# Optimization experiments

Measured on AMD Instinct MI355X. Metric: run time of the kernel, lower is better.

## Reference

```python
import jax, jax.numpy as jnp
import numpy as np
import math

MAXL = 2
N = 256
TAU = 8


def _cg_coeff(j1, m1, j2, m2, J, M):
    if m1 + m2 != M or J < abs(j1 - j2) or J > j1 + j2:
        return 0.0
    f = math.factorial
    pre = math.sqrt((2 * J + 1) * f(J + j1 - j2) * f(J - j1 + j2) * f(j1 + j2 - J) / f(j1 + j2 + J + 1))
    pre *= math.sqrt(f(J + M) * f(J - M) * f(j1 - m1) * f(j1 + m1) * f(j2 - m2) * f(j2 + m2))
    kmin = max(0, j2 - J - m1, j1 + m2 - J)
    kmax = min(j1 + j2 - J, j1 - m1, j2 + m2)
    s = 0.0
    for k in range(kmin, kmax + 1):
        s += (-1.0) ** k / (f(k) * f(j1 + j2 - J - k) * f(j1 - m1 - k) * f(j2 + m2 - k) * f(J - j2 + m1 + k) * f(J - j1 - m2 + k))
    return pre * s


def _cg_tensor(l1, l2, L):
    C = np.zeros((2 * l1 + 1, 2 * l2 + 1, 2 * L + 1), np.float32)
    for m1 in range(-l1, l1 + 1):
        for m2 in range(-l2, l2 + 1):
            M = m1 + m2
            if -L <= M <= L:
                C[m1 + l1, m2 + l2, M + L] = _cg_coeff(l1, m1, l2, m2, L, M)
    return C

_CG = {}
for _l1 in range(MAXL + 1):
    for _l2 in range(MAXL + 1):
        for _L in range(abs(_l1 - _l2), min(_l1 + _l2, MAXL) + 1):
            _CG[(_l1, _l2, _L)] = _cg_tensor(_l1, _l2, _L)


def _cgproduct(xs, ys, maxl):
    # xs[l]: [..., 2l+1, tau_x], ys[l]: [..., 2l+1, tau_y]
    out = []
    for L in range(maxl + 1):
        chunks = []
        for l1 in range(maxl + 1):
            for l2 in range(maxl + 1):
                if abs(l1 - l2) <= L <= l1 + l2:
                    C = jnp.asarray(_CG[(l1, l2, L)])
                    t = jnp.einsum('...mc,...nd,mnM->...Mcd', xs[l1], ys[l2], C)
                    sh = t.shape
                    chunks.append(t.reshape(sh[:-2] + (sh[-2] * sh[-1],)))
        out.append(jnp.concatenate(chunks, axis=-1))
    return out


def _forward(v0, v1, v2, adj, s0, s1, s2, wn0, wn1, wn2, wr0, wr1, wr2):
    v = [v0, v1, v2]                       # [N, 1, 2l+1, tau]
    sph = [s0[None], s1[None], s2[None]]   # [1, N, N, 2l+1, 1]
    wn = [wn0, wn1, wn2]
    wr = [wr0, wr1, wr2]
    # message pass: gather/sum over neighbors (Rmask1 gather)
    vmp = [jnp.einsum('ij,jamc->iamc', adj, p)[None] for p in v]  # [1, N, 1, 2l+1, tau]
    # first CG product (vertex x vertex)
    cg_nl = _cgproduct(vmp, vmp, MAXL)
    # per-l channel mixing with weights_nl
    mixed = [jnp.einsum('bxymc,cd->bxymd', cg_nl[l], wn[l]) for l in range(MAXL + 1)]
    # repeat to pairwise adims [N, N] (broadcast over second array dim)
    n = adj.shape[0]
    rep = [jnp.broadcast_to(m, (1, n, n, m.shape[3], m.shape[4])) for m in mixed]
    # second CG product with relative-position spherical harmonics
    cg_rel = _cgproduct(rep, sph, MAXL)
    # per-cell mixing with weights_rel
    mixed_rel = [jnp.einsum('bxymc,xycd->bxymd', cg_rel[l], wr[l]) for l in range(MAXL + 1)]
    # sum over source-node array dim
    vsum = [jnp.sum(m, axis=1) for m in mixed_rel]  # [1, N, 2l+1, tau]
    # NormalizeVecArr mutates parts in place -> returned vertices_sum is normalized
    out = [p / jnp.sum(p) for p in vsum]
    # concatenate parts along m-axis for a single output array [1, N, 9, tau]
    return jnp.concatenate(out, axis=2)


def setup_inputs() -> dict:
    key = jax.random.key(0)
    ks = jax.random.split(key, 13)
    d = {}
    d['v0'] = jax.random.normal(ks[0], (N, 1, 1, TAU), jnp.float32)
    d['v1'] = jax.random.normal(ks[1], (N, 1, 3, TAU), jnp.float32)
    d['v2'] = jax.random.normal(ks[2], (N, 1, 5, TAU), jnp.float32)
    d['adj'] = jax.random.uniform(ks[3], (N, N), jnp.float32)
    d['s0'] = jax.random.normal(ks[4], (N, N, 1, 1), jnp.float32)
    d['s1'] = jax.random.normal(ks[5], (N, N, 3, 1), jnp.float32)
    d['s2'] = jax.random.normal(ks[6], (N, N, 5, 1), jnp.float32)
    W = 0.05
    d['wn0'] = W * jax.random.normal(ks[7], (192, TAU), jnp.float32)
    d['wn1'] = W * jax.random.normal(ks[8], (384, TAU), jnp.float32)
    d['wn2'] = W * jax.random.normal(ks[9], (384, TAU), jnp.float32)
    d['wr0'] = W * jax.random.normal(ks[10], (N, N, 24, TAU), jnp.float32)
    d['wr1'] = W * jax.random.normal(ks[11], (N, N, 48, TAU), jnp.float32)
    d['wr2'] = W * jax.random.normal(ks[12], (N, N, 48, TAU), jnp.float32)
    return d


def reference(v0, v1, v2, adj, s0, s1, s2, wn0, wn1, wn2, wr0, wr1, wr2):
    return _forward(v0, v1, v2, adj, s0, s1, s2, wn0, wn1, wn2, wr0, wr1, wr2)
```

## Files before the change

kernel.cpp:

```cpp
#include <hip/hip_runtime.h>

#define NN 256

#define C13  0.5773502691896258f
#define C15  0.4472135954999579f
#define CC12 0.7071067811865476f
#define S35  0.7745966692414834f
#define S310 0.5477225575051661f
#define C110 0.3162277660168379f
#define S25  0.6324555320336759f
#define S23  0.8164965809277260f
#define C16  0.4082482904638630f
#define S27  0.5345224838248488f
#define S37  0.6546536707079771f
#define C114 0.2672612419124244f

#define CGREL(mx, sv, r0, r1, r2) \
    r0[0] = mx[0]*sv[0]; \
    r0[1] = C13*(mx[1]*sv[3] - mx[2]*sv[2] + mx[3]*sv[1]); \
    r0[2] = C15*(mx[4]*sv[8] - mx[5]*sv[7] + mx[6]*sv[6] - mx[7]*sv[5] + mx[8]*sv[4]); \
    r1[0][0] = mx[0]*sv[1]; r1[1][0] = mx[0]*sv[2]; r1[2][0] = mx[0]*sv[3]; \
    r1[0][1] = mx[1]*sv[0]; r1[1][1] = mx[2]*sv[0]; r1[2][1] = mx[3]*sv[0]; \
    r1[0][2] = CC12*(mx[2]*sv[1] - mx[1]*sv[2]); \
    r1[1][2] = CC12*(mx[3]*sv[1] - mx[1]*sv[3]); \
    r1[2][2] = CC12*(mx[3]*sv[2] - mx[2]*sv[3]); \
    r1[0][3] = S35*mx[3]*sv[4] - S310*mx[2]*sv[5] + C110*mx[1]*sv[6]; \
    r1[1][3] = S310*(mx[3]*sv[5] + mx[1]*sv[7]) - S25*mx[2]*sv[6]; \
    r1[2][3] = S35*mx[1]*sv[8] - S310*mx[2]*sv[7] + C110*mx[3]*sv[6]; \
    r1[0][4] = C110*mx[6]*sv[1] - S310*mx[5]*sv[2] + S35*mx[4]*sv[3]; \
    r1[1][4] = S310*(mx[7]*sv[1] + mx[5]*sv[3]) - S25*mx[6]*sv[2]; \
    r1[2][4] = S35*mx[8]*sv[1] - S310*mx[7]*sv[2] + C110*mx[6]*sv[3]; \
    r1[0][5] = C15*(mx[7]*sv[4] - mx[4]*sv[7]) + S310*(mx[5]*sv[6] - mx[6]*sv[5]); \
    r1[1][5] = S25*(mx[8]*sv[4] - mx[4]*sv[8]) + C110*(mx[5]*sv[7] - mx[7]*sv[5]); \
    r1[2][5] = C15*(mx[8]*sv[5] - mx[5]*sv[8]) + S310*(mx[6]*sv[7] - mx[7]*sv[6]); \
    r2[0][0]=mx[0]*sv[4]; r2[1][0]=mx[0]*sv[5]; r2[2][0]=mx[0]*sv[6]; r2[3][0]=mx[0]*sv[7]; r2[4][0]=mx[0]*sv[8]; \
    r2[0][1] = mx[1]*sv[1]; \
    r2[1][1] = CC12*(mx[2]*sv[1] + mx[1]*sv[2]); \
    r2[2][1] = C16*(mx[3]*sv[1] + mx[1]*sv[3]) + S23*mx[2]*sv[2]; \
    r2[3][1] = CC12*(mx[3]*sv[2] + mx[2]*sv[3]); \
    r2[4][1] = mx[3]*sv[3]; \
    r2[0][2] = S23*mx[2]*sv[4] - C13*mx[1]*sv[5]; \
    r2[1][2] = C13*mx[3]*sv[4] + C16*mx[2]*sv[5] - CC12*mx[1]*sv[6]; \
    r2[2][2] = CC12*(mx[3]*sv[5] - mx[1]*sv[7]); \
    r2[3][2] = CC12*mx[3]*sv[6] - C16*mx[2]*sv[7] - C13*mx[1]*sv[8]; \
    r2[4][2] = C13*mx[3]*sv[7] - S23*mx[2]*sv[8]; \
    r2[0][3]=mx[4]*sv[0]; r2[1][3]=mx[5]*sv[0]; r2[2][3]=mx[6]*sv[0]; r2[3][3]=mx[7]*sv[0]; r2[4][3]=mx[8]*sv[0]; \
    r2[0][4] = C13*mx[5]*sv[1] - S23*mx[4]*sv[2]; \
    r2[1][4] = CC12*mx[6]*sv[1] - C16*mx[5]*sv[2] - C13*mx[4]*sv[3]; \
    r2[2][4] = CC12*(mx[7]*sv[1] - mx[5]*sv[3]); \
    r2[3][4] = C13*mx[8]*sv[1] + C16*mx[7]*sv[2] - CC12*mx[6]*sv[3]; \
    r2[4][4] = S23*mx[8]*sv[2] - C13*mx[7]*sv[3]; \
    r2[0][5] = S27*(mx[4]*sv[6] + mx[6]*sv[4]) - S37*mx[5]*sv[5]; \
    r2[1][5] = S37*(mx[4]*sv[7] + mx[7]*sv[4]) - C114*(mx[5]*sv[6] + mx[6]*sv[5]); \
    r2[2][5] = S27*(mx[8]*sv[4] + mx[4]*sv[8] - mx[6]*sv[6]) + C114*(mx[7]*sv[5] + mx[5]*sv[7]); \
    r2[3][5] = S37*(mx[8]*sv[5] + mx[5]*sv[8]) - C114*(mx[7]*sv[6] + mx[6]*sv[7]); \
    r2[4][5] = S27*(mx[8]*sv[6] + mx[6]*sv[8]) - S37*mx[7]*sv[7];

__global__ __launch_bounds__(256) void k_nodes(
                        const float* __restrict__ adj,
                        const float* __restrict__ v0,
                        const float* __restrict__ v1,
                        const float* __restrict__ v2,
                        const float* __restrict__ wn0,
                        const float* __restrict__ wn1,
                        const float* __restrict__ wn2,
                        float* __restrict__ mixed){
  __shared__ float part[4][72];
  int i = blockIdx.x;
  int tid = threadIdx.x, wv = tid >> 6, lane = tid & 63;

  {
    const float* vp1; int st1;
    if (lane < 8)       { vp1 = v0 + lane;      st1 = 8;  }
    else if (lane < 32) { vp1 = v1 + (lane-8);  st1 = 24; }
    else                { vp1 = v2 + (lane-32); st1 = 40; }
    const float* vp2 = v2 + 32 + lane;
    const float* arow = adj + i*NN;
    int j0 = wv*64;
    float a1a = 0.f, a1b = 0.f, a2a = 0.f, a2b = 0.f;
    #pragma unroll 8
    for (int j = j0; j < j0+64; j += 2){
      float av0 = arow[j], av1 = arow[j+1];
      a1a = fmaf(av0, vp1[j*st1], a1a);
      a1b = fmaf(av1, vp1[(j+1)*st1], a1b);
      if (lane < 8){
        a2a = fmaf(av0, vp2[j*40], a2a);
        a2b = fmaf(av1, vp2[(j+1)*40], a2b);
      }
    }
    part[wv][lane] = a1a + a1b;
    if (lane < 8) part[wv][64+lane] = a2a + a2b;
  }
  __syncthreads();
  if (wv) return;

  {
    float s = part[0][lane] + part[1][lane] + part[2][lane] + part[3][lane];
    float s2 = 0.f;
    if (lane < 8)
      s2 = part[0][64+lane] + part[1][64+lane] + part[2][64+lane] + part[3][64+lane];
    part[0][lane] = s;
    if (lane < 8) part[0][64+lane] = s2;
  }

  int c = lane >> 3, d = lane & 7;
  float mx[9], sv[9];
  #pragma unroll
  for (int j=0;j<9;j++){ mx[j] = part[0][j*8 + c]; sv[j] = part[0][j*8 + d]; }
  float r0[3], r1[3][6], r2[5][6];
  CGREL(mx, sv, r0, r1, r2)

  float a0[8], a1m[3][8], a2m[5][8];
  #pragma unroll
  for (int dp=0;dp<8;dp++){ a0[dp]=0.f;
    #pragma unroll
    for (int M=0;M<3;M++) a1m[M][dp]=0.f;
    #pragma unroll
    for (int M=0;M<5;M++) a2m[M][dp]=0.f;
  }
  #pragma unroll
  for (int k=0;k<3;k++){
    const float* row = wn0 + (k*64 + lane)*8;
    float4 u = *(const float4*)row;
    float4 v = *(const float4*)(row+4);
    float u8[8] = {u.x,u.y,u.z,u.w,v.x,v.y,v.z,v.w};
    #pragma unroll
    for (int dp=0;dp<8;dp++) a0[dp] = fmaf(r0[k], u8[dp], a0[dp]);
  }
  #pragma unroll
  for (int k=0;k<6;k++){
    const float* row = wn1 + (k*64 + lane)*8;
    float4 u = *(const float4*)row;
    float4 v = *(const float4*)(row+4);
    float u8[8] = {u.x,u.y,u.z,u.w,v.x,v.y,v.z,v.w};
    #pragma unroll
    for (int M=0;M<3;M++)
      #pragma unroll
      for (int dp=0;dp<8;dp++) a1m[M][dp] = fmaf(r1[M][k], u8[dp], a1m[M][dp]);
  }
  #pragma unroll
  for (int k=0;k<6;k++){
    const float* row = wn2 + (k*64 + lane)*8;
    float4 u = *(const float4*)row;
    float4 v = *(const float4*)(row+4);
    float u8[8] = {u.x,u.y,u.z,u.w,v.x,v.y,v.z,v.w};
    #pragma unroll
    for (int M=0;M<5;M++)
      #pragma unroll
      for (int dp=0;dp<8;dp++) a2m[M][dp] = fmaf(r2[M][k], u8[dp], a2m[M][dp]);
  }

  #pragma unroll
  for (int m=0;m<9;m++){
    #pragma unroll
    for (int dp=0;dp<8;dp++){
      float val = (m==0) ? a0[dp] : (m<4 ? a1m[m-1][dp] : a2m[m-4][dp]);
      val += __shfl_xor(val, 1);
      val += __shfl_xor(val, 2);
      val += __shfl_xor(val, 4);
      val += __shfl_xor(val, 8);
      val += __shfl_xor(val, 16);
      val += __shfl_xor(val, 32);
      if (lane == ((m*8+dp) & 63)) mixed[i*72 + m*8 + dp] = val;
    }
  }
}

#define XPW 8

#define LOAD_WR(x, W0, W1, W2) { \
  int pxy = (x)*NN + y; \
  const float* p0 = wr0 + pxy*192 + lane; \
  const float* p1 = wr1 + pxy*384 + lane; \
  const float* p2 = wr2 + pxy*384 + lane; \
  _Pragma("unroll") for (int k=0;k<3;k++) W0[k] = p0[k*64]; \
  _Pragma("unroll") for (int k=0;k<6;k++) W1[k] = p1[k*64]; \
  _Pragma("unroll") for (int k=0;k<6;k++) W2[k] = p2[k*64]; }

#define LOAD_MS(x) { \
  const float* mb = mixed + (x)*72 + cgp; \
  _Pragma("unroll") for (int j=0;j<9;j++) mx[j] = mb[j*8]; \
  int pxy = (x)*NN + y; \
  sv[0] = s0[pxy]; \
  _Pragma("unroll") for (int j=0;j<3;j++) sv[1+j] = s1[pxy*3+j]; \
  _Pragma("unroll") for (int j=0;j<5;j++) sv[4+j] = s2[pxy*5+j]; }

#define DO_FMA(W0, W1, W2) { \
  _Pragma("unroll") for (int k=0;k<3;k++) acc[0] = fmaf(r0[k], W0[k], acc[0]); \
  _Pragma("unroll") for (int k=0;k<6;k++){ \
    acc[1] = fmaf(r1[0][k], W1[k], acc[1]); \
    acc[2] = fmaf(r1[1][k], W1[k], acc[2]); \
    acc[3] = fmaf(r1[2][k], W1[k], acc[3]); \
    acc[4] = fmaf(r2[0][k], W2[k], acc[4]); \
    acc[5] = fmaf(r2[1][k], W2[k], acc[5]); \
    acc[6] = fmaf(r2[2][k], W2[k], acc[6]); \
    acc[7] = fmaf(r2[3][k], W2[k], acc[7]); \
    acc[8] = fmaf(r2[4][k], W2[k], acc[8]); } }

#define STEP(xw, WC0, WC1, WC2, WN0, WN1, WN2, xm) { \
  LOAD_WR(xw, WN0, WN1, WN2); \
  float r0[3], r1[3][6], r2[5][6]; \
  CGREL(mx, sv, r0, r1, r2) \
  LOAD_MS(xm); \
  DO_FMA(WC0, WC1, WC2); }

__global__ __launch_bounds__(256, 4) void k_pair(
    const float* __restrict__ mixed,
    const float* __restrict__ s0, const float* __restrict__ s1, const float* __restrict__ s2,
    const float* __restrict__ wr0, const float* __restrict__ wr1, const float* __restrict__ wr2,
    float* __restrict__ vsum){
  int tid = threadIdx.x;
  int lane = tid & 63;
  int w = blockIdx.x*4 + (tid>>6);
  int y = w & (NN-1);
  int xbase = (w >> 8) * XPW;
  int cgp = lane >> 3;
  int xlast = xbase + XPW - 1;

  float acc[9];
  #pragma unroll
  for (int m=0;m<9;m++) acc[m]=0.f;

  float mx[9], sv[9];
  float wA0[3], wA1[6], wA2[6], wB0[3], wB1[6], wB2[6];
  LOAD_MS(xbase);
  LOAD_WR(xbase, wA0, wA1, wA2);

  #pragma unroll
  for (int i=0;i<XPW;i+=2){
    int x1 = xbase + i + 1;
    int x2 = (i+2 < XPW) ? (xbase + i + 2) : xlast;
    STEP(x1, wA0, wA1, wA2, wB0, wB1, wB2, x1);
    STEP(x2, wB0, wB1, wB2, wA0, wA1, wA2, x2);
  }

  #pragma unroll
  for (int m=0;m<9;m++){
    float v = acc[m];
    v += __shfl_xor(v, 8);
    v += __shfl_xor(v, 16);
    v += __shfl_xor(v, 32);
    acc[m] = v;
  }
  if (lane < 8){
    #pragma unroll
    for (int m=0;m<9;m++) atomicAdd(&vsum[y*72 + m*8 + lane], acc[m]);
  }
}

__global__ void k_final(const float* __restrict__ vsum, float* __restrict__ out){
  __shared__ float ps[3];
  int t = threadIdx.x;
  if (t < 3) ps[t] = 0.f;
  __syncthreads();
  float vals[18];
  float p0=0.f, p1=0.f, p2=0.f;
  #pragma unroll
  for (int k=0;k<18;k++){
    int idx = t*18 + k;
    float v = vsum[idx];
    vals[k] = v;
    int mall = (idx >> 3) % 9;
    if (mall == 0) p0 += v; else if (mall < 4) p1 += v; else p2 += v;
  }
  #pragma unroll
  for (int s=1; s<64; s<<=1){
    p0 += __shfl_xor(p0, s);
    p1 += __shfl_xor(p1, s);
    p2 += __shfl_xor(p2, s);
  }
  if ((t & 63) == 0){
    atomicAdd(&ps[0], p0);
    atomicAdd(&ps[1], p1);
    atomicAdd(&ps[2], p2);
  }
  __syncthreads();
  float q0 = ps[0], q1 = ps[1], q2 = ps[2];
  #pragma unroll
  for (int k=0;k<18;k++){
    int idx = t*18 + k;
    int mall = (idx >> 3) % 9;
    float den = (mall == 0) ? q0 : (mall < 4 ? q1 : q2);
    out[idx] = vals[k] / den;
  }
}

extern "C" void kernel_launch(void* const* d_in, const int* in_sizes, int n_in,
                              void* d_out, int out_size, void* d_ws, size_t ws_size,
                              hipStream_t stream) {
  const float* v0  = (const float*)d_in[0];
  const float* v1  = (const float*)d_in[1];
  const float* v2  = (const float*)d_in[2];
  const float* adj = (const float*)d_in[3];
  const float* s0  = (const float*)d_in[4];
  const float* s1  = (const float*)d_in[5];
  const float* s2  = (const float*)d_in[6];
  const float* wn0 = (const float*)d_in[7];
  const float* wn1 = (const float*)d_in[8];
  const float* wn2 = (const float*)d_in[9];
  const float* wr0 = (const float*)d_in[10];
  const float* wr1 = (const float*)d_in[11];
  const float* wr2 = (const float*)d_in[12];
  float* out = (float*)d_out;

  float* ws    = (float*)d_ws;
  float* mixed = ws;
  float* vsum  = ws + 18432;

  hipMemsetAsync(vsum, 0, 18432*sizeof(float), stream);
  k_nodes<<<NN, 256, 0, stream>>>(adj, v0, v1, v2, wn0, wn1, wn2, mixed);
  k_pair<<<NN*(NN/XPW)/4, 256, 0, stream>>>(mixed, s0, s1, s2, wr0, wr1, wr2, vsum);
  k_final<<<1, 1024, 0, stream>>>(vsum, out);
}
```

Before: 83.83 us.

## Stream pair weights into a per-wave LDS ring via async global-to-LDS loads

Rewrites k_pair so each wave stages its mixed features, spherical harmonics and per-pair wr weights into shared memory with global_load_lds. The wr loads go through a three-deep ring buffer controlled by explicit vmcnt waits and scheduling barriers, replacing the register double-buffering. The aim is to keep more weight bytes in flight to hide the latency of this bandwidth-bound stream. In exchange it uses about 58KB of LDS per block, which limits occupancy, and drops the launch-bounds occupancy hint. It also depends on hand-counted waitcnt values and on LDS reads finishing before the async refills of the same slot.

```diff
diff --git a/kernel.cpp b/kernel.cpp
--- a/kernel.cpp
+++ b/kernel.cpp
@@ -1,6 +1,8 @@
 #include <hip/hip_runtime.h>
 
 #define NN 256
+#define XPW 8
+#define RING_D 3
 
 #define C13  0.5773502691896258f
 #define C15  0.4472135954999579f
@@ -56,6 +58,12 @@
     r2[3][5] = S37*(mx[8]*sv[5] + mx[5]*sv[8]) - C114*(mx[7]*sv[6] + mx[6]*sv[7]); \
     r2[4][5] = S27*(mx[8]*sv[6] + mx[6]*sv[8]) - S37*mx[7]*sv[7];
 
+typedef __attribute__((address_space(3))) unsigned       lds_u32_t;
+typedef __attribute__((address_space(1))) const unsigned glb_u32_t;
+__device__ __forceinline__ void gld4(const float* g, float* l){
+  __builtin_amdgcn_global_load_lds((glb_u32_t*)g, (lds_u32_t*)l, 4, 0, 0);
+}
+
 __global__ __launch_bounds__(256) void k_nodes(
                         const float* __restrict__ adj,
                         const float* __restrict__ v0,
@@ -68,7 +76,6 @@
   __shared__ float part[4][72];
   int i = blockIdx.x;
   int tid = threadIdx.x, wv = tid >> 6, lane = tid & 63;
-
   {
     const float* vp1; int st1;
     if (lane < 8)       { vp1 = v0 + lane;      st1 = 8;  }
@@ -93,7 +100,6 @@
   }
   __syncthreads();
   if (wv) return;
-
   {
     float s = part[0][lane] + part[1][lane] + part[2][lane] + part[3][lane];
     float s2 = 0.f;
@@ -102,7 +108,6 @@
     part[0][lane] = s;
     if (lane < 8) part[0][64+lane] = s2;
   }
-
   int c = lane >> 3, d = lane & 7;
   float mx[9], sv[9];
   #pragma unroll
@@ -149,7 +154,6 @@
       #pragma unroll
       for (int dp=0;dp<8;dp++) a2m[M][dp] = fmaf(r2[M][k], u8[dp], a2m[M][dp]);
   }
-
   #pragma unroll
   for (int m=0;m<9;m++){
     #pragma unroll
@@ -166,73 +170,99 @@
   }
 }
 
-#define XPW 8
-
-#define LOAD_WR(x, W0, W1, W2) { \
-  int pxy = (x)*NN + y; \
-  const float* p0 = wr0 + pxy*192 + lane; \
-  const float* p1 = wr1 + pxy*384 + lane; \
-  const float* p2 = wr2 + pxy*384 + lane; \
-  _Pragma("unroll") for (int k=0;k<3;k++) W0[k] = p0[k*64]; \
-  _Pragma("unroll") for (int k=0;k<6;k++) W1[k] = p1[k*64]; \
-  _Pragma("unroll") for (int k=0;k<6;k++) W2[k] = p2[k*64]; }
-
-#define LOAD_MS(x) { \
-  const float* mb = mixed + (x)*72 + cgp; \
-  _Pragma("unroll") for (int j=0;j<9;j++) mx[j] = mb[j*8]; \
-  int pxy = (x)*NN + y; \
-  sv[0] = s0[pxy]; \
-  _Pragma("unroll") for (int j=0;j<3;j++) sv[1+j] = s1[pxy*3+j]; \
-  _Pragma("unroll") for (int j=0;j<5;j++) sv[4+j] = s2[pxy*5+j]; }
-
-#define DO_FMA(W0, W1, W2) { \
-  _Pragma("unroll") for (int k=0;k<3;k++) acc[0] = fmaf(r0[k], W0[k], acc[0]); \
-  _Pragma("unroll") for (int k=0;k<6;k++){ \
-    acc[1] = fmaf(r1[0][k], W1[k], acc[1]); \
-    acc[2] = fmaf(r1[1][k], W1[k], acc[2]); \
-    acc[3] = fmaf(r1[2][k], W1[k], acc[3]); \
-    acc[4] = fmaf(r2[0][k], W2[k], acc[4]); \
-    acc[5] = fmaf(r2[1][k], W2[k], acc[5]); \
-    acc[6] = fmaf(r2[2][k], W2[k], acc[6]); \
-    acc[7] = fmaf(r2[3][k], W2[k], acc[7]); \
-    acc[8] = fmaf(r2[4][k], W2[k], acc[8]); } }
-
-#define STEP(xw, WC0, WC1, WC2, WN0, WN1, WN2, xm) { \
-  LOAD_WR(xw, WN0, WN1, WN2); \
+#define WAVE_F 3648
+
+__device__ __forceinline__ void prefetch_pair(
+    int x, int y, int lane,
+    const float* __restrict__ wr0, const float* __restrict__ wr1,
+    const float* __restrict__ wr2, float* slotp){
+  int pxy = x*NN + y;
+  const float* g0 = wr0 + (size_t)pxy*192 + lane;
+  const float* g1 = wr1 + (size_t)pxy*384 + lane;
+  const float* g2 = wr2 + (size_t)pxy*384 + lane;
+  #pragma unroll
+  for (int k=0;k<3;k++) gld4(g0 + k*64, slotp + k*64);
+  #pragma unroll
+  for (int k=0;k<6;k++) gld4(g1 + k*64, slotp + 192 + k*64);
+  #pragma unroll
+  for (int k=0;k<6;k++) gld4(g2 + k*64, slotp + 576 + k*64);
+}
+
+#define CONSUME(iIdx, slotIdx) { \
+  const float* slotp = Lw + (slotIdx)*960; \
+  float w0v[3], w1v[6], w2v[6]; \
+  _Pragma("unroll") for (int k=0;k<3;k++) w0v[k] = slotp[k*64 + lane]; \
+  _Pragma("unroll") for (int k=0;k<6;k++) w1v[k] = slotp[192 + k*64 + lane]; \
+  _Pragma("unroll") for (int k=0;k<6;k++) w2v[k] = slotp[576 + k*64 + lane]; \
+  const float* mixp = Lw + 2880 + (iIdx)*72; \
+  float mx[9], sv[9]; \
+  _Pragma("unroll") for (int j=0;j<9;j++) mx[j] = mixp[j*8 + cgp]; \
+  sv[0] = Lw[3456 + (iIdx)]; \
+  _Pragma("unroll") for (int j=0;j<3;j++) sv[1+j] = Lw[3520 + (iIdx)*3 + j]; \
+  _Pragma("unroll") for (int j=0;j<5;j++) sv[4+j] = Lw[3584 + (iIdx)*5 + j]; \
   float r0[3], r1[3][6], r2[5][6]; \
   CGREL(mx, sv, r0, r1, r2) \
-  LOAD_MS(xm); \
-  DO_FMA(WC0, WC1, WC2); }
-
-__global__ __launch_bounds__(256, 4) void k_pair(
+  _Pragma("unroll") for (int k=0;k<3;k++) acc[0] = fmaf(r0[k], w0v[k], acc[0]); \
+  _Pragma("unroll") for (int k=0;k<6;k++){ \
+    acc[1] = fmaf(r1[0][k], w1v[k], acc[1]); \
+    acc[2] = fmaf(r1[1][k], w1v[k], acc[2]); \
+    acc[3] = fmaf(r1[2][k], w1v[k], acc[3]); \
+    acc[4] = fmaf(r2[0][k], w2v[k], acc[4]); \
+    acc[5] = fmaf(r2[1][k], w2v[k], acc[5]); \
+    acc[6] = fmaf(r2[2][k], w2v[k], acc[6]); \
+    acc[7] = fmaf(r2[3][k], w2v[k], acc[7]); \
+    acc[8] = fmaf(r2[4][k], w2v[k], acc[8]); } }
+
+#define WAITVM(n) { \
+  asm volatile("s_waitcnt vmcnt(" #n ")" ::: "memory"); \
+  __builtin_amdgcn_sched_barrier(0); }
+
+__global__ __launch_bounds__(256) void k_pair(
     const float* __restrict__ mixed,
     const float* __restrict__ s0, const float* __restrict__ s1, const float* __restrict__ s2,
     const float* __restrict__ wr0, const float* __restrict__ wr1, const float* __restrict__ wr2,
     float* __restrict__ vsum){
+  __shared__ float L[4][WAVE_F];
   int tid = threadIdx.x;
   int lane = tid & 63;
-  int w = blockIdx.x*4 + (tid>>6);
+  int wv = tid >> 6;
+  int w = blockIdx.x*4 + wv;
   int y = w & (NN-1);
   int xbase = (w >> 8) * XPW;
   int cgp = lane >> 3;
-  int xlast = xbase + XPW - 1;
+  float* Lw = &L[wv][0];
+
+  {
+    #pragma unroll
+    for (int t=0;t<9;t++)
+      gld4(mixed + xbase*72 + t*64 + lane, Lw + 2880 + t*64);
+    gld4(s0 + (xbase + (lane & 7))*NN + y, Lw + 3456);
+    { int e = lane < 24 ? lane : 23; int si = e/3, sj = e - si*3;
+      gld4(s1 + ((size_t)((xbase+si)*NN + y))*3 + sj, Lw + 3520); }
+    { int e = lane < 40 ? lane : 39; int si = e/5, sj = e - si*5;
+      gld4(s2 + ((size_t)((xbase+si)*NN + y))*5 + sj, Lw + 3584); }
+    #pragma unroll
+    for (int p=0;p<RING_D;p++)
+      prefetch_pair(xbase + p, y, lane, wr0, wr1, wr2, Lw + p*960);
+  }
 
   float acc[9];
   #pragma unroll
   for (int m=0;m<9;m++) acc[m]=0.f;
 
-  float mx[9], sv[9];
-  float wA0[3], wA1[6], wA2[6], wB0[3], wB1[6], wB2[6];
-  LOAD_MS(xbase);
-  LOAD_WR(xbase, wA0, wA1, wA2);
-
-  #pragma unroll
-  for (int i=0;i<XPW;i+=2){
-    int x1 = xbase + i + 1;
-    int x2 = (i+2 < XPW) ? (xbase + i + 2) : xlast;
-    STEP(x1, wA0, wA1, wA2, wB0, wB1, wB2, x1);
-    STEP(x2, wB0, wB1, wB2, wA0, wA1, wA2, x2);
-  }
+  int slot = 0;
+  for (int i=0;i<XPW-2;i++){
+    WAITVM(30)
+    CONSUME(i, slot);
+    if (i < XPW-RING_D)
+      prefetch_pair(xbase + i + RING_D, y, lane, wr0, wr1, wr2, Lw + slot*960);
+    slot = (slot == RING_D-1) ? 0 : slot+1;
+  }
+  WAITVM(15)
+  CONSUME(XPW-2, slot);
+  slot = (slot == RING_D-1) ? 0 : slot+1;
+  WAITVM(0)
+  CONSUME(XPW-1, slot);
 
   #pragma unroll
   for (int m=0;m<9;m++){
```

Result: slower. 92.39 us (+10.2%).
